# Kernel tuning notes

Measured on AMD Instinct MI355X. Metric: run time of the kernel, lower is better.

The kernel has to match this reference:

```python
import jax, jax.numpy as jnp
import numpy as np


def setup_inputs() -> dict:
    key = jax.random.key(0)
    k1, k2, k3 = jax.random.split(key, 3)
    B, IN, OUT, NCLS = 16384, 512, 1024, 5
    inputs = jax.random.normal(k1, (B, IN), dtype=jnp.float32)
    centres = jax.random.normal(k2, (OUT, IN), dtype=jnp.float32)  # nn.init.normal_(0,1)
    log_sigmas = jnp.zeros((OUT,), dtype=jnp.float32)  # constant_(0)
    # nn.Linear(out_features, 5) default init: U(-1/sqrt(fan_in), 1/sqrt(fan_in))
    bound = 1.0 / np.sqrt(OUT)
    fc_w = jax.random.uniform(k3, (NCLS, OUT), dtype=jnp.float32, minval=-bound, maxval=bound)
    fc_b = jnp.zeros((NCLS,), dtype=jnp.float32)
    return {"inputs": inputs, "centres": centres, "log_sigmas": log_sigmas,
            "fc_w": fc_w, "fc_b": fc_b}


def reference(inputs, centres, log_sigmas, fc_w, fc_b):
    # avoiding the (B, out, in) expanded intermediate the torch code builds.
    x2 = jnp.sum(inputs * inputs, axis=-1, keepdims=True)          # [B, 1]
    c2 = jnp.sum(centres * centres, axis=-1)                       # [O]
    sq = x2 + c2[None, :] - 2.0 * jnp.einsum('bi,oi->bo', inputs, centres)
    sq = jnp.maximum(sq, 0.0)                                      # [B, O]
    # distances = sqrt(sq) / exp(log_sigmas); basis = exp(-distances^2)
    dist = jnp.sqrt(sq) / jnp.exp(log_sigmas)[None, :]
    basis = jnp.exp(-(dist * dist))                                # [B, O]
    return jnp.einsum('bo,no->bn', basis, fc_w) + fc_b             # [B, 5]
```

## Files before the change

kernel.cpp:

```cpp
#include <hip/hip_runtime.h>
#include <hip/hip_bf16.h>
#include <cmath>

#define NB 16384
#define NK 512
#define NO 1024
#define NC 5
#define NSL 16

typedef float f32x4 __attribute__((ext_vector_type(4)));
typedef short s16x8 __attribute__((ext_vector_type(8)));

__device__ inline short f2bf(float f) {
    union { __hip_bfloat16 h; short s; } u;
    u.h = __float2bfloat16(f);
    return u.s;
}

__global__ void prep_bf16(const float* __restrict__ x, const float* __restrict__ c,
                          short* __restrict__ xbf, short* __restrict__ cbf,
                          float* __restrict__ x2, float* __restrict__ c2) {
    int gw   = (blockIdx.x * blockDim.x + threadIdx.x) >> 6;
    int lane = threadIdx.x & 63;
    if (gw >= NB + NO) return;
    bool isX = gw < NB;
    const float* src = isX ? (x + (size_t)gw * NK) : (c + (size_t)(gw - NB) * NK);
    short*       dst = isX ? (xbf + (size_t)gw * NK) : (cbf + (size_t)(gw - NB) * NK);
    f32x4 v0 = *(const f32x4*)(src + lane * 8);
    f32x4 v1 = *(const f32x4*)(src + lane * 8 + 4);
    s16x8 o;
    float s = 0.f;
#pragma unroll
    for (int j = 0; j < 4; ++j) {
        s += v0[j] * v0[j] + v1[j] * v1[j];
        o[j]     = f2bf(v0[j]);
        o[4 + j] = f2bf(v1[j]);
    }
    *(s16x8*)(dst + lane * 8) = o;
#pragma unroll
    for (int off = 1; off < 64; off <<= 1) s += __shfl_xor(s, off);
    if (lane == 0) {
        if (isX) x2[gw] = s;
        else     c2[gw - NB] = s;
    }
}

__global__ void prep_f32(const float* __restrict__ x, const float* __restrict__ c,
                         float* __restrict__ x2, float* __restrict__ c2) {
    int gw   = (blockIdx.x * blockDim.x + threadIdx.x) >> 6;
    int lane = threadIdx.x & 63;
    if (gw >= NB + NO) return;
    const float* src = (gw < NB) ? (x + (size_t)gw * NK)
                                 : (c + (size_t)(gw - NB) * NK);
    f32x4 v0 = *(const f32x4*)(src + lane * 8);
    f32x4 v1 = *(const f32x4*)(src + lane * 8 + 4);
    float s = 0.f;
#pragma unroll
    for (int j = 0; j < 4; ++j) s += v0[j] * v0[j] + v1[j] * v1[j];
#pragma unroll
    for (int off = 1; off < 64; off <<= 1) s += __shfl_xor(s, off);
    if (lane == 0) {
        if (gw < NB) x2[gw] = s;
        else         c2[gw - NB] = s;
    }
}

__global__ void init_out(float* __restrict__ out, const float* __restrict__ fcb) {
    int i = blockIdx.x * blockDim.x + threadIdx.x;
    if (i < NB * NC) out[i] = fcb[i % NC];
}

__global__ void reduce_out(const float* __restrict__ part,
                           const float* __restrict__ fcb,
                           float* __restrict__ out) {
    int i = blockIdx.x * blockDim.x + threadIdx.x;
    if (i >= NB * NC / 4) return;
    f32x4 s = {0.f, 0.f, 0.f, 0.f};
#pragma unroll
    for (int sl = 0; sl < NSL; ++sl)
        s += *(const f32x4*)(part + (size_t)sl * NB * NC + i * 4);
    f32x4 o;
#pragma unroll
    for (int j = 0; j < 4; ++j) o[j] = s[j] + fcb[(i * 4 + j) % NC];
    *(f32x4*)(out + i * 4) = o;
}

__device__ inline void rbf_epilogue_part(f32x4 acc[4][4],
                                         const float* __restrict__ x2,
                                         const float* __restrict__ c2,
                                         const float* __restrict__ ls,
                                         const float* __restrict__ fcw,
                                         float* __restrict__ part,
                                         int bm, int bn, int wr, int wc,
                                         int lc, int kg) {
    const int growb0 = bm * 128 + wr * 64 + kg * 4;
    const int gcol0  = bn * 128 + wc * 64 + lc;
    float* slice = part + (size_t)(bn * 2 + wc) * NB * NC;

    float c2v[4], invs2[4], w[4][5];
#pragma unroll
    for (int ni = 0; ni < 4; ++ni) {
        int gc = gcol0 + ni * 16;
        c2v[ni]   = c2[gc];
        invs2[ni] = expf(-2.f * ls[gc]);
#pragma unroll
        for (int n = 0; n < 5; ++n) w[ni][n] = fcw[n * NO + gc];
    }

#pragma unroll
    for (int mi = 0; mi < 4; ++mi) {
        float rs[4][5];
#pragma unroll
        for (int r = 0; r < 4; ++r)
#pragma unroll
            for (int n = 0; n < 5; ++n) rs[r][n] = 0.f;

#pragma unroll
        for (int r = 0; r < 4; ++r) {
            float x2v = x2[growb0 + mi * 16 + r];
#pragma unroll
            for (int ni = 0; ni < 4; ++ni) {
                float sq    = fmaxf(x2v + c2v[ni] - 2.f * acc[mi][ni][r], 0.f);
                float basis = expf(-sq * invs2[ni]);
#pragma unroll
                for (int n = 0; n < 5; ++n) rs[r][n] += basis * w[ni][n];
            }
        }
#pragma unroll
        for (int off = 1; off < 16; off <<= 1)
#pragma unroll
            for (int r = 0; r < 4; ++r)
#pragma unroll
                for (int n = 0; n < 5; ++n) rs[r][n] += __shfl_xor(rs[r][n], off);

        if (lc == 0) {
            float* dst = slice + (size_t)(growb0 + mi * 16) * NC;
            f32x4 v0 = {rs[0][0], rs[0][1], rs[0][2], rs[0][3]};
            f32x4 v1 = {rs[0][4], rs[1][0], rs[1][1], rs[1][2]};
            f32x4 v2 = {rs[1][3], rs[1][4], rs[2][0], rs[2][1]};
            f32x4 v3 = {rs[2][2], rs[2][3], rs[2][4], rs[3][0]};
            f32x4 v4 = {rs[3][1], rs[3][2], rs[3][3], rs[3][4]};
            *(f32x4*)(dst)      = v0;
            *(f32x4*)(dst + 4)  = v1;
            *(f32x4*)(dst + 8)  = v2;
            *(f32x4*)(dst + 12) = v3;
            *(f32x4*)(dst + 16) = v4;
        }
    }
}

__device__ inline void rbf_epilogue_atomic(f32x4 acc[4][4],
                                           const float* __restrict__ x2,
                                           const float* __restrict__ c2,
                                           const float* __restrict__ ls,
                                           const float* __restrict__ fcw,
                                           float* __restrict__ out,
                                           int bm, int bn, int wr, int wc,
                                           int lc, int kg) {
    const int growb0 = bm * 128 + wr * 64 + kg * 4;
    const int gcol0  = bn * 128 + wc * 64 + lc;
    float c2v[4], invs2[4], w[4][5];
#pragma unroll
    for (int ni = 0; ni < 4; ++ni) {
        int gc = gcol0 + ni * 16;
        c2v[ni]   = c2[gc];
        invs2[ni] = expf(-2.f * ls[gc]);
#pragma unroll
        for (int n = 0; n < 5; ++n) w[ni][n] = fcw[n * NO + gc];
    }
#pragma unroll
    for (int mi = 0; mi < 4; ++mi) {
        float rs[4][5];
#pragma unroll
        for (int r = 0; r < 4; ++r)
#pragma unroll
            for (int n = 0; n < 5; ++n) rs[r][n] = 0.f;
#pragma unroll
        for (int r = 0; r < 4; ++r) {
            float x2v = x2[growb0 + mi * 16 + r];
#pragma unroll
            for (int ni = 0; ni < 4; ++ni) {
                float sq    = fmaxf(x2v + c2v[ni] - 2.f * acc[mi][ni][r], 0.f);
                float basis = expf(-sq * invs2[ni]);
#pragma unroll
                for (int n = 0; n < 5; ++n) rs[r][n] += basis * w[ni][n];
            }
        }
#pragma unroll
        for (int off = 1; off < 16; off <<= 1)
#pragma unroll
            for (int r = 0; r < 4; ++r)
#pragma unroll
                for (int n = 0; n < 5; ++n) rs[r][n] += __shfl_xor(rs[r][n], off);
        if (lc == 0) {
#pragma unroll
            for (int r = 0; r < 4; ++r) {
                int grow = growb0 + mi * 16 + r;
#pragma unroll
                for (int n = 0; n < 5; ++n)
                    atomicAdd(&out[(size_t)grow * NC + n], rs[r][n]);
            }
        }
    }
}

__global__ __launch_bounds__(256)
void rbf_gemm_bf16(const short* __restrict__ Abf, const short* __restrict__ Bbf,
                   const float* __restrict__ x2, const float* __restrict__ c2,
                   const float* __restrict__ ls, const float* __restrict__ fcw,
                   float* __restrict__ part) {
    __shared__ short As[2][128 * 32];
    __shared__ short Bs[2][128 * 32];

    const int t    = threadIdx.x;
    const int lane = t & 63, wave = t >> 6;
    const int wr = wave >> 1, wc = wave & 1;
    const int lc = lane & 15, kg = lane >> 4;

    const int orig = blockIdx.x;
    const int wg   = (orig >> 3) + (orig & 7) * (1024 / 8);
    const int bm = wg >> 3, bn = wg & 7;

    const int srow = wave * 16 + (lane >> 2);
    const int scol = (lane & 3) * 8;
    const short* gA = Abf + (size_t)(bm * 128 + srow) * NK + scol;
    const short* gB = Bbf + (size_t)(bn * 128 + srow) * NK + scol;

#define STAGE(buf, kt)                                                          \
    _Pragma("unroll")                                                           \
    for (int j = 0; j < 2; ++j) {                                               \
        __builtin_amdgcn_global_load_lds(                                       \
            (const __attribute__((address_space(1))) unsigned int*)(gA + (size_t)j * 64 * NK + (kt) * 32), \
            (__attribute__((address_space(3))) unsigned int*)(&As[buf][wave * 512 + j * 2048]), \
            16, 0, 0);                                                          \
        __builtin_amdgcn_global_load_lds(                                       \
            (const __attribute__((address_space(1))) unsigned int*)(gB + (size_t)j * 64 * NK + (kt) * 32), \
            (__attribute__((address_space(3))) unsigned int*)(&Bs[buf][wave * 512 + j * 2048]), \
            16, 0, 0);                                                          \
    }

    f32x4 acc[4][4];
#pragma unroll
    for (int i = 0; i < 4; ++i)
#pragma unroll
        for (int j = 0; j < 4; ++j)
#pragma unroll
            for (int k = 0; k < 4; ++k) acc[i][j][k] = 0.f;

    const int aoff = (wr * 64 + lc) * 32 + kg * 8;
    const int boff = (wc * 64 + lc) * 32 + kg * 8;

#define COMPUTE(buf)                                                            \
    {                                                                           \
        s16x8 af[4], bfv[4];                                                    \
        _Pragma("unroll")                                                       \
        for (int mi = 0; mi < 4; ++mi) af[mi]  = *(const s16x8*)(&As[buf][aoff + mi * 512]); \
        _Pragma("unroll")                                                       \
        for (int ni = 0; ni < 4; ++ni) bfv[ni] = *(const s16x8*)(&Bs[buf][boff + ni * 512]); \
        _Pragma("unroll")                                                       \
        for (int mi = 0; mi < 4; ++mi)                                          \
            _Pragma("unroll")                                                   \
            for (int ni = 0; ni < 4; ++ni)                                      \
                acc[mi][ni] = __builtin_amdgcn_mfma_f32_16x16x32_bf16(          \
                    af[mi], bfv[ni], acc[mi][ni], 0, 0, 0);                     \
    }

    STAGE(0, 0);
    __syncthreads();
    for (int kt = 0; kt < NK / 32; kt += 2) {
        STAGE(1, kt + 1);
        COMPUTE(0);
        __syncthreads();
        if (kt + 2 < NK / 32) STAGE(0, kt + 2);
        COMPUTE(1);
        __syncthreads();
    }
#undef STAGE
#undef COMPUTE

    rbf_epilogue_part(acc, x2, c2, ls, fcw, part, bm, bn, wr, wc, lc, kg);
}

__global__ __launch_bounds__(256)
void rbf_gemm_f32(const float* __restrict__ X, const float* __restrict__ Cn,
                  const float* __restrict__ x2, const float* __restrict__ c2,
                  const float* __restrict__ ls, const float* __restrict__ fcw,
                  float* __restrict__ out) {
    __shared__ short As[128 * 40];
    __shared__ short Bs[128 * 40];

    const int t    = threadIdx.x;
    const int lane = t & 63, wave = t >> 6;
    const int wr = wave >> 1, wc = wave & 1;
    const int lc = lane & 15, kg = lane >> 4;
    const int bn = blockIdx.x & 7, bm = blockIdx.x >> 3;

    const int srow = t >> 1, shalf = t & 1;
    const float* pA = X  + (size_t)(bm * 128 + srow) * NK + shalf * 16;
    const float* pB = Cn + (size_t)(bn * 128 + srow) * NK + shalf * 16;
    const int sbase = srow * 40 + shalf * 16;

    f32x4 ra[4], rb[4];
#pragma unroll
    for (int i = 0; i < 4; ++i) {
        ra[i] = *(const f32x4*)(pA + i * 4);
        rb[i] = *(const f32x4*)(pB + i * 4);
    }

    f32x4 acc[4][4];
#pragma unroll
    for (int i = 0; i < 4; ++i)
#pragma unroll
        for (int j = 0; j < 4; ++j)
#pragma unroll
            for (int k = 0; k < 4; ++k) acc[i][j][k] = 0.f;

    const short* Ab = As + (wr * 64 + lc) * 40 + kg * 8;
    const short* Bb = Bs + (wc * 64 + lc) * 40 + kg * 8;

    for (int kt = 0; kt < NK / 32; ++kt) {
        __syncthreads();
        s16x8 va0, va1, vb0, vb1;
#pragma unroll
        for (int i = 0; i < 8; ++i) {
            va0[i] = f2bf(ra[i >> 2][i & 3]);
            va1[i] = f2bf(ra[2 + (i >> 2)][i & 3]);
            vb0[i] = f2bf(rb[i >> 2][i & 3]);
            vb1[i] = f2bf(rb[2 + (i >> 2)][i & 3]);
        }
        *(s16x8*)&As[sbase]     = va0;
        *(s16x8*)&As[sbase + 8] = va1;
        *(s16x8*)&Bs[sbase]     = vb0;
        *(s16x8*)&Bs[sbase + 8] = vb1;
        __syncthreads();

        if (kt + 1 < NK / 32) {
            const float* qA = pA + (kt + 1) * 32;
            const float* qB = pB + (kt + 1) * 32;
#pragma unroll
            for (int i = 0; i < 4; ++i) {
                ra[i] = *(const f32x4*)(qA + i * 4);
                rb[i] = *(const f32x4*)(qB + i * 4);
            }
        }

        s16x8 af[4], bfv[4];
#pragma unroll
        for (int mi = 0; mi < 4; ++mi) af[mi]  = *(const s16x8*)(Ab + mi * 16 * 40);
#pragma unroll
        for (int ni = 0; ni < 4; ++ni) bfv[ni] = *(const s16x8*)(Bb + ni * 16 * 40);
#pragma unroll
        for (int mi = 0; mi < 4; ++mi)
#pragma unroll
            for (int ni = 0; ni < 4; ++ni)
                acc[mi][ni] = __builtin_amdgcn_mfma_f32_16x16x32_bf16(
                    af[mi], bfv[ni], acc[mi][ni], 0, 0, 0);
    }

    rbf_epilogue_atomic(acc, x2, c2, ls, fcw, out, bm, bn, wr, wc, lc, kg);
}

extern "C" void kernel_launch(void* const* d_in, const int* in_sizes, int n_in,
                              void* d_out, int out_size, void* d_ws, size_t ws_size,
                              hipStream_t stream) {
    const float* X   = (const float*)d_in[0];
    const float* Cn  = (const float*)d_in[1];
    const float* ls  = (const float*)d_in[2];
    const float* fcw = (const float*)d_in[3];
    const float* fcb = (const float*)d_in[4];
    float* out = (float*)d_out;

    const size_t xbf_e  = (size_t)NB * NK;
    const size_t cbf_e  = (size_t)NO * NK;
    const size_t part_e = (size_t)NSL * NB * NC;
    const size_t need   = (xbf_e + cbf_e) * 2 + (NB + NO) * 4 + part_e * 4;

    if (ws_size >= need) {
        short* xbf  = (short*)d_ws;
        short* cbf  = xbf + xbf_e;
        float* x2   = (float*)(cbf + cbf_e);
        float* c2   = x2 + NB;
        float* part = c2 + NO;
        prep_bf16<<<(NB + NO + 3) / 4, 256, 0, stream>>>(X, Cn, xbf, cbf, x2, c2);
        rbf_gemm_bf16<<<(NO / 128) * (NB / 128), 256, 0, stream>>>(xbf, cbf, x2, c2, ls, fcw, part);
        reduce_out<<<(NB * NC / 4 + 255) / 256, 256, 0, stream>>>(part, fcb, out);
    } else {
        float* x2 = (float*)d_ws;
        float* c2 = x2 + NB;
        init_out<<<(NB * NC + 255) / 256, 256, 0, stream>>>(out, fcb);
        prep_f32<<<(NB + NO + 3) / 4, 256, 0, stream>>>(X, Cn, x2, c2);
        rbf_gemm_f32<<<(NO / 128) * (NB / 128), 256, 0, stream>>>(X, Cn, x2, c2, ls, fcw, out);
    }
}
```

Before: 130.0 us.

## Switch RBF GEMM to 256x256 tiles with 4-stage LDS pipeline

Replaces the 128x128, 4-wave, double-buffered bf16 GEMM with a 256x256-tile, 8-wave kernel that uses four LDS buffers, interleaves global-to-LDS staging with the MFMA phases, and raises wave priority around the MFMA blocks. It also XOR-swizzles the LDS layout to avoid bank conflicts and remaps workgroups for L2 locality. The epilogue is folded in and writes 16 partial slices, 4 per column block. Larger tiles cut global and LDS traffic per FLOP and the deeper pipeline hides load latency, at the cost of more registers and LDS per block, which limits occupancy.

```diff
diff --git a/kernel.cpp b/kernel.cpp
--- a/kernel.cpp
+++ b/kernel.cpp
@@ -7,6 +7,7 @@
 #define NO 1024
 #define NC 5
 #define NSL 16
+#define NT 16
 
 typedef float f32x4 __attribute__((ext_vector_type(4)));
 typedef short s16x8 __attribute__((ext_vector_type(8)));
@@ -85,17 +86,116 @@
     *(f32x4*)(out + i * 4) = o;
 }
 
-__device__ inline void rbf_epilogue_part(f32x4 acc[4][4],
-                                         const float* __restrict__ x2,
-                                         const float* __restrict__ c2,
-                                         const float* __restrict__ ls,
-                                         const float* __restrict__ fcw,
-                                         float* __restrict__ part,
-                                         int bm, int bn, int wr, int wc,
-                                         int lc, int kg) {
-    const int growb0 = bm * 128 + wr * 64 + kg * 4;
-    const int gcol0  = bn * 128 + wc * 64 + lc;
-    float* slice = part + (size_t)(bn * 2 + wc) * NB * NC;
+__global__ __launch_bounds__(512, 2)
+void rbf_gemm_256(const short* __restrict__ Abf, const short* __restrict__ Bbf,
+                  const float* __restrict__ x2, const float* __restrict__ c2,
+                  const float* __restrict__ ls, const float* __restrict__ fcw,
+                  float* __restrict__ part) {
+    __shared__ short As[4][256 * 32];
+    __shared__ short Bs[4][256 * 32];
+
+    const int t    = threadIdx.x;
+    const int lane = t & 63, wave = t >> 6;
+    const int wr  = wave >> 2, wcn = wave & 3;
+    const int lr  = lane & 15, kg  = lane >> 4;
+
+    const int orig = blockIdx.x;
+    const int wg   = (orig & 7) * 32 + (orig >> 3);
+    const int bm = wg >> 2, bn = wg & 3;
+
+    const int tc   = t ^ ((t >> 3) & 1);
+    const int srow = tc >> 2;
+    const int scol = (tc & 3) * 8;
+    const short* gA = Abf + (size_t)(bm * 256 + srow) * NK + scol;
+    const short* gB = Bbf + (size_t)(bn * 256 + srow) * NK + scol;
+
+    const int akoff = (kg * 8) ^ ((lane & 2) << 2);
+    const int arow0 = wr * 128 + lr;
+    const int brow0 = wcn * 64 + lr;
+
+    f32x4 acc[8][4];
+#pragma unroll
+    for (int i = 0; i < 8; ++i)
+#pragma unroll
+        for (int j = 0; j < 4; ++j)
+#pragma unroll
+            for (int k = 0; k < 4; ++k) acc[i][j][k] = 0.f;
+
+#define STAGE_A(kt)                                                             \
+    _Pragma("unroll")                                                           \
+    for (int j = 0; j < 2; ++j)                                                 \
+        __builtin_amdgcn_global_load_lds(                                       \
+            (const __attribute__((address_space(1))) unsigned int*)(gA + (size_t)j * 128 * NK + (kt) * 32), \
+            (__attribute__((address_space(3))) unsigned int*)(&As[(kt) & 3][j * 4096 + wave * 512]), \
+            16, 0, 0);
+
+#define STAGE_B(kt)                                                             \
+    _Pragma("unroll")                                                           \
+    for (int j = 0; j < 2; ++j)                                                 \
+        __builtin_amdgcn_global_load_lds(                                       \
+            (const __attribute__((address_space(1))) unsigned int*)(gB + (size_t)j * 128 * NK + (kt) * 32), \
+            (__attribute__((address_space(3))) unsigned int*)(&Bs[(kt) & 3][j * 4096 + wave * 512]), \
+            16, 0, 0);
+
+#define TILE_BODY(b, kt2, DOSTAGE)                                              \
+    {                                                                           \
+        const short* Ab = &As[b][0];                                            \
+        const short* Bb = &Bs[b][0];                                            \
+        s16x8 bfr[4], afr[4];                                                   \
+        _Pragma("unroll")                                                       \
+        for (int ni = 0; ni < 4; ++ni)                                          \
+            bfr[ni] = *(const s16x8*)(Bb + (brow0 + ni * 16) * 32 + akoff);     \
+        _Pragma("unroll")                                                       \
+        for (int mi = 0; mi < 4; ++mi)                                          \
+            afr[mi] = *(const s16x8*)(Ab + (arow0 + mi * 16) * 32 + akoff);     \
+        if (DOSTAGE) { STAGE_A(kt2); }                                          \
+        __builtin_amdgcn_s_setprio(1);                                          \
+        _Pragma("unroll")                                                       \
+        for (int mi = 0; mi < 4; ++mi)                                          \
+            _Pragma("unroll")                                                   \
+            for (int ni = 0; ni < 4; ++ni)                                      \
+                acc[mi][ni] = __builtin_amdgcn_mfma_f32_16x16x32_bf16(          \
+                    afr[mi], bfr[ni], acc[mi][ni], 0, 0, 0);                    \
+        __builtin_amdgcn_s_setprio(0);                                          \
+        _Pragma("unroll")                                                       \
+        for (int mi = 0; mi < 4; ++mi)                                          \
+            afr[mi] = *(const s16x8*)(Ab + (arow0 + (mi + 4) * 16) * 32 + akoff); \
+        if (DOSTAGE) { STAGE_B(kt2); }                                          \
+        __builtin_amdgcn_s_setprio(1);                                          \
+        _Pragma("unroll")                                                       \
+        for (int mi = 0; mi < 4; ++mi)                                          \
+            _Pragma("unroll")                                                   \
+            for (int ni = 0; ni < 4; ++ni)                                      \
+                acc[mi + 4][ni] = __builtin_amdgcn_mfma_f32_16x16x32_bf16(      \
+                    afr[mi], bfr[ni], acc[mi + 4][ni], 0, 0, 0);                \
+        __builtin_amdgcn_s_setprio(0);                                          \
+    }
+
+    STAGE_A(0); STAGE_B(0);
+    STAGE_A(1); STAGE_B(1);
+    asm volatile("s_waitcnt vmcnt(4)" ::: "memory");
+    __builtin_amdgcn_s_barrier();
+    __builtin_amdgcn_sched_barrier(0);
+
+    for (int kt = 0; kt < NT - 2; ++kt) {
+        TILE_BODY(kt & 3, kt + 2, true);
+        asm volatile("s_waitcnt vmcnt(4)" ::: "memory");
+        __builtin_amdgcn_s_barrier();
+        __builtin_amdgcn_sched_barrier(0);
+    }
+    TILE_BODY((NT - 2) & 3, 0, false);
+    asm volatile("s_waitcnt vmcnt(0)" ::: "memory");
+    __builtin_amdgcn_s_barrier();
+    __builtin_amdgcn_sched_barrier(0);
+    TILE_BODY((NT - 1) & 3, 0, false);
+
+#undef TILE_BODY
+#undef STAGE_A
+#undef STAGE_B
+
+    const int growb0 = bm * 256 + wr * 128 + kg * 4;
+    const int gcol0  = bn * 256 + wcn * 64 + lr;
+    float* slice = part + (size_t)(bn * 4 + wcn) * NB * NC;
 
     float c2v[4], invs2[4], w[4][5];
 #pragma unroll
@@ -108,7 +208,7 @@
     }
 
 #pragma unroll
-    for (int mi = 0; mi < 4; ++mi) {
+    for (int mi = 0; mi < 8; ++mi) {
         float rs[4][5];
 #pragma unroll
         for (int r = 0; r < 4; ++r)
@@ -133,7 +233,7 @@
 #pragma unroll
                 for (int n = 0; n < 5; ++n) rs[r][n] += __shfl_xor(rs[r][n], off);
 
-        if (lc == 0) {
+        if (lr == 0) {
             float* dst = slice + (size_t)(growb0 + mi * 16) * NC;
             f32x4 v0 = {rs[0][0], rs[0][1], rs[0][2], rs[0][3]};
             f32x4 v1 = {rs[0][4], rs[1][0], rs[1][1], rs[1][2]};
@@ -205,83 +305,6 @@
 }
 
 __global__ __launch_bounds__(256)
-void rbf_gemm_bf16(const short* __restrict__ Abf, const short* __restrict__ Bbf,
-                   const float* __restrict__ x2, const float* __restrict__ c2,
-                   const float* __restrict__ ls, const float* __restrict__ fcw,
-                   float* __restrict__ part) {
-    __shared__ short As[2][128 * 32];
-    __shared__ short Bs[2][128 * 32];
-
-    const int t    = threadIdx.x;
-    const int lane = t & 63, wave = t >> 6;
-    const int wr = wave >> 1, wc = wave & 1;
-    const int lc = lane & 15, kg = lane >> 4;
-
-    const int orig = blockIdx.x;
-    const int wg   = (orig >> 3) + (orig & 7) * (1024 / 8);
-    const int bm = wg >> 3, bn = wg & 7;
-
-    const int srow = wave * 16 + (lane >> 2);
-    const int scol = (lane & 3) * 8;
-    const short* gA = Abf + (size_t)(bm * 128 + srow) * NK + scol;
-    const short* gB = Bbf + (size_t)(bn * 128 + srow) * NK + scol;
-
-#define STAGE(buf, kt)                                                          \
-    _Pragma("unroll")                                                           \
-    for (int j = 0; j < 2; ++j) {                                               \
-        __builtin_amdgcn_global_load_lds(                                       \
-            (const __attribute__((address_space(1))) unsigned int*)(gA + (size_t)j * 64 * NK + (kt) * 32), \
-            (__attribute__((address_space(3))) unsigned int*)(&As[buf][wave * 512 + j * 2048]), \
-            16, 0, 0);                                                          \
-        __builtin_amdgcn_global_load_lds(                                       \
-            (const __attribute__((address_space(1))) unsigned int*)(gB + (size_t)j * 64 * NK + (kt) * 32), \
-            (__attribute__((address_space(3))) unsigned int*)(&Bs[buf][wave * 512 + j * 2048]), \
-            16, 0, 0);                                                          \
-    }
-
-    f32x4 acc[4][4];
-#pragma unroll
-    for (int i = 0; i < 4; ++i)
-#pragma unroll
-        for (int j = 0; j < 4; ++j)
-#pragma unroll
-            for (int k = 0; k < 4; ++k) acc[i][j][k] = 0.f;
-
-    const int aoff = (wr * 64 + lc) * 32 + kg * 8;
-    const int boff = (wc * 64 + lc) * 32 + kg * 8;
-
-#define COMPUTE(buf)                                                            \
-    {                                                                           \
-        s16x8 af[4], bfv[4];                                                    \
-        _Pragma("unroll")                                                       \
-        for (int mi = 0; mi < 4; ++mi) af[mi]  = *(const s16x8*)(&As[buf][aoff + mi * 512]); \
-        _Pragma("unroll")                                                       \
-        for (int ni = 0; ni < 4; ++ni) bfv[ni] = *(const s16x8*)(&Bs[buf][boff + ni * 512]); \
-        _Pragma("unroll")                                                       \
-        for (int mi = 0; mi < 4; ++mi)                                          \
-            _Pragma("unroll")                                                   \
-            for (int ni = 0; ni < 4; ++ni)                                      \
-                acc[mi][ni] = __builtin_amdgcn_mfma_f32_16x16x32_bf16(          \
-                    af[mi], bfv[ni], acc[mi][ni], 0, 0, 0);                     \
-    }
-
-    STAGE(0, 0);
-    __syncthreads();
-    for (int kt = 0; kt < NK / 32; kt += 2) {
-        STAGE(1, kt + 1);
-        COMPUTE(0);
-        __syncthreads();
-        if (kt + 2 < NK / 32) STAGE(0, kt + 2);
-        COMPUTE(1);
-        __syncthreads();
-    }
-#undef STAGE
-#undef COMPUTE
-
-    rbf_epilogue_part(acc, x2, c2, ls, fcw, part, bm, bn, wr, wc, lc, kg);
-}
-
-__global__ __launch_bounds__(256)
 void rbf_gemm_f32(const float* __restrict__ X, const float* __restrict__ Cn,
                   const float* __restrict__ x2, const float* __restrict__ c2,
                   const float* __restrict__ ls, const float* __restrict__ fcw,
@@ -382,7 +405,7 @@
         float* c2   = x2 + NB;
         float* part = c2 + NO;
         prep_bf16<<<(NB + NO + 3) / 4, 256, 0, stream>>>(X, Cn, xbf, cbf, x2, c2);
-        rbf_gemm_bf16<<<(NO / 128) * (NB / 128), 256, 0, stream>>>(xbf, cbf, x2, c2, ls, fcw, part);
+        rbf_gemm_256<<<(NB / 256) * (NO / 256), 512, 0, stream>>>(xbf, cbf, x2, c2, ls, fcw, part);
         reduce_out<<<(NB * NC / 4 + 255) / 256, 256, 0, stream>>>(part, fcb, out);
     } else {
         float* x2 = (float*)d_ws;
```

Measured after the change: 122.6 us. 5.7% less time.

## Use 256x128 block tile with 512 threads, swizzled LDS and MFMA priority

Applied to the files above, without the earlier changes.

Replaces the 128x128, 256-thread bf16 GEMM with a 256x128 tile run by 8 waves, so each B tile is loaded once for twice as many rows. The LDS load addresses are XOR-swizzled to cut bank conflicts, and s_setprio is raised around the MFMA block. The loop uses a single-barrier double-buffered schedule with a different workgroup remapping. The fused RBF epilogue is inlined into the new kernel. Larger blocks halve the grid and may reduce occupancy or hurt load balance.

```diff
diff --git a/kernel.cpp b/kernel.cpp
--- a/kernel.cpp
+++ b/kernel.cpp
@@ -7,9 +7,12 @@
 #define NO 1024
 #define NC 5
 #define NSL 16
+#define NT 16
 
 typedef float f32x4 __attribute__((ext_vector_type(4)));
 typedef short s16x8 __attribute__((ext_vector_type(8)));
+#define AS1 __attribute__((address_space(1)))
+#define AS3 __attribute__((address_space(3)))
 
 __device__ inline short f2bf(float f) {
     union { __hip_bfloat16 h; short s; } u;
@@ -85,17 +88,83 @@
     *(f32x4*)(out + i * 4) = o;
 }
 
-__device__ inline void rbf_epilogue_part(f32x4 acc[4][4],
-                                         const float* __restrict__ x2,
-                                         const float* __restrict__ c2,
-                                         const float* __restrict__ ls,
-                                         const float* __restrict__ fcw,
-                                         float* __restrict__ part,
-                                         int bm, int bn, int wr, int wc,
-                                         int lc, int kg) {
-    const int growb0 = bm * 128 + wr * 64 + kg * 4;
-    const int gcol0  = bn * 128 + wc * 64 + lc;
-    float* slice = part + (size_t)(bn * 2 + wc) * NB * NC;
+__global__ __launch_bounds__(512, 4)
+void rbf_gemm_512(const short* __restrict__ Abf, const short* __restrict__ Bbf,
+                  const float* __restrict__ x2, const float* __restrict__ c2,
+                  const float* __restrict__ ls, const float* __restrict__ fcw,
+                  float* __restrict__ part) {
+    __shared__ short As[2][256 * 32];
+    __shared__ short Bs[2][128 * 32];
+
+    const int t    = threadIdx.x;
+    const int lane = t & 63;
+    const int wave = t >> 6;
+    const int wr   = wave >> 1, wcn = wave & 1;
+    const int lr   = lane & 15, kg  = lane >> 4;
+
+    const int orig = blockIdx.x;
+    const int wg   = (orig & 7) * 64 + (orig >> 3);
+    const int bm = wg >> 3, bn = wg & 7;
+
+    const int l0   = t ^ ((t >> 3) & 3);
+    const int srow = l0 >> 2;
+    const int kc8  = (l0 & 3) * 8;
+    const short* gA0 = Abf + (size_t)(bm * 256 + srow) * NK + kc8;
+    const short* gA1 = gA0 + (size_t)128 * NK;
+    const short* gB0 = Bbf + (size_t)(bn * 128 + srow) * NK + kc8;
+
+#define STAGE(buf, kt) do {                                                     \
+    __builtin_amdgcn_global_load_lds(                                           \
+        (const AS1 unsigned int*)(gA0 + (kt) * 32),                             \
+        (AS3 unsigned int*)(&As[buf][(size_t)t * 8]), 16, 0, 0);                \
+    __builtin_amdgcn_global_load_lds(                                           \
+        (const AS1 unsigned int*)(gA1 + (kt) * 32),                             \
+        (AS3 unsigned int*)(&As[buf][(size_t)(512 + t) * 8]), 16, 0, 0);        \
+    __builtin_amdgcn_global_load_lds(                                           \
+        (const AS1 unsigned int*)(gB0 + (kt) * 32),                             \
+        (AS3 unsigned int*)(&Bs[buf][(size_t)t * 8]), 16, 0, 0);                \
+} while (0)
+
+    const int akoff = (kg ^ ((lr >> 1) & 3)) * 8;
+    const int arow0 = (wr * 64 + lr) * 32;
+    const int brow0 = (wcn * 64 + lr) * 32;
+
+    f32x4 acc[4][4];
+#pragma unroll
+    for (int i = 0; i < 4; ++i)
+#pragma unroll
+        for (int j = 0; j < 4; ++j)
+#pragma unroll
+            for (int k = 0; k < 4; ++k) acc[i][j][k] = 0.f;
+
+    STAGE(0, 0);
+    __syncthreads();
+#pragma unroll
+    for (int kt = 0; kt < NT; ++kt) {
+        const int buf = kt & 1;
+        if (kt + 1 < NT) STAGE(buf ^ 1, kt + 1);
+        s16x8 af[4], bfv[4];
+#pragma unroll
+        for (int ni = 0; ni < 4; ++ni)
+            bfv[ni] = *(const s16x8*)(&Bs[buf][brow0 + ni * 512 + akoff]);
+#pragma unroll
+        for (int mi = 0; mi < 4; ++mi)
+            af[mi]  = *(const s16x8*)(&As[buf][arow0 + mi * 512 + akoff]);
+        __builtin_amdgcn_s_setprio(1);
+#pragma unroll
+        for (int mi = 0; mi < 4; ++mi)
+#pragma unroll
+            for (int ni = 0; ni < 4; ++ni)
+                acc[mi][ni] = __builtin_amdgcn_mfma_f32_16x16x32_bf16(
+                    af[mi], bfv[ni], acc[mi][ni], 0, 0, 0);
+        __builtin_amdgcn_s_setprio(0);
+        if (kt + 1 < NT) __syncthreads();
+    }
+#undef STAGE
+
+    const int growb0 = bm * 256 + wr * 64 + kg * 4;
+    const int gcol0  = bn * 128 + wcn * 64 + lr;
+    float* slice = part + (size_t)(bn * 2 + wcn) * NB * NC;
 
     float c2v[4], invs2[4], w[4][5];
 #pragma unroll
@@ -133,7 +202,7 @@
 #pragma unroll
                 for (int n = 0; n < 5; ++n) rs[r][n] += __shfl_xor(rs[r][n], off);
 
-        if (lc == 0) {
+        if (lr == 0) {
             float* dst = slice + (size_t)(growb0 + mi * 16) * NC;
             f32x4 v0 = {rs[0][0], rs[0][1], rs[0][2], rs[0][3]};
             f32x4 v1 = {rs[0][4], rs[1][0], rs[1][1], rs[1][2]};
@@ -205,83 +274,6 @@
 }
 
 __global__ __launch_bounds__(256)
-void rbf_gemm_bf16(const short* __restrict__ Abf, const short* __restrict__ Bbf,
-                   const float* __restrict__ x2, const float* __restrict__ c2,
-                   const float* __restrict__ ls, const float* __restrict__ fcw,
-                   float* __restrict__ part) {
-    __shared__ short As[2][128 * 32];
-    __shared__ short Bs[2][128 * 32];
-
-    const int t    = threadIdx.x;
-    const int lane = t & 63, wave = t >> 6;
-    const int wr = wave >> 1, wc = wave & 1;
-    const int lc = lane & 15, kg = lane >> 4;
-
-    const int orig = blockIdx.x;
-    const int wg   = (orig >> 3) + (orig & 7) * (1024 / 8);
-    const int bm = wg >> 3, bn = wg & 7;
-
-    const int srow = wave * 16 + (lane >> 2);
-    const int scol = (lane & 3) * 8;
-    const short* gA = Abf + (size_t)(bm * 128 + srow) * NK + scol;
-    const short* gB = Bbf + (size_t)(bn * 128 + srow) * NK + scol;
-
-#define STAGE(buf, kt)                                                          \
-    _Pragma("unroll")                                                           \
-    for (int j = 0; j < 2; ++j) {                                               \
-        __builtin_amdgcn_global_load_lds(                                       \
-            (const __attribute__((address_space(1))) unsigned int*)(gA + (size_t)j * 64 * NK + (kt) * 32), \
-            (__attribute__((address_space(3))) unsigned int*)(&As[buf][wave * 512 + j * 2048]), \
-            16, 0, 0);                                                          \
-        __builtin_amdgcn_global_load_lds(                                       \
-            (const __attribute__((address_space(1))) unsigned int*)(gB + (size_t)j * 64 * NK + (kt) * 32), \
-            (__attribute__((address_space(3))) unsigned int*)(&Bs[buf][wave * 512 + j * 2048]), \
-            16, 0, 0);                                                          \
-    }
-
-    f32x4 acc[4][4];
-#pragma unroll
-    for (int i = 0; i < 4; ++i)
-#pragma unroll
-        for (int j = 0; j < 4; ++j)
-#pragma unroll
-            for (int k = 0; k < 4; ++k) acc[i][j][k] = 0.f;
-
-    const int aoff = (wr * 64 + lc) * 32 + kg * 8;
-    const int boff = (wc * 64 + lc) * 32 + kg * 8;
-
-#define COMPUTE(buf)                                                            \
-    {                                                                           \
-        s16x8 af[4], bfv[4];                                                    \
-        _Pragma("unroll")                                                       \
-        for (int mi = 0; mi < 4; ++mi) af[mi]  = *(const s16x8*)(&As[buf][aoff + mi * 512]); \
-        _Pragma("unroll")                                                       \
-        for (int ni = 0; ni < 4; ++ni) bfv[ni] = *(const s16x8*)(&Bs[buf][boff + ni * 512]); \
-        _Pragma("unroll")                                                       \
-        for (int mi = 0; mi < 4; ++mi)                                          \
-            _Pragma("unroll")                                                   \
-            for (int ni = 0; ni < 4; ++ni)                                      \
-                acc[mi][ni] = __builtin_amdgcn_mfma_f32_16x16x32_bf16(          \
-                    af[mi], bfv[ni], acc[mi][ni], 0, 0, 0);                     \
-    }
-
-    STAGE(0, 0);
-    __syncthreads();
-    for (int kt = 0; kt < NK / 32; kt += 2) {
-        STAGE(1, kt + 1);
-        COMPUTE(0);
-        __syncthreads();
-        if (kt + 2 < NK / 32) STAGE(0, kt + 2);
-        COMPUTE(1);
-        __syncthreads();
-    }
-#undef STAGE
-#undef COMPUTE
-
-    rbf_epilogue_part(acc, x2, c2, ls, fcw, part, bm, bn, wr, wc, lc, kg);
-}
-
-__global__ __launch_bounds__(256)
 void rbf_gemm_f32(const float* __restrict__ X, const float* __restrict__ Cn,
                   const float* __restrict__ x2, const float* __restrict__ c2,
                   const float* __restrict__ ls, const float* __restrict__ fcw,
@@ -382,7 +374,7 @@
         float* c2   = x2 + NB;
         float* part = c2 + NO;
         prep_bf16<<<(NB + NO + 3) / 4, 256, 0, stream>>>(X, Cn, xbf, cbf, x2, c2);
-        rbf_gemm_bf16<<<(NO / 128) * (NB / 128), 256, 0, stream>>>(xbf, cbf, x2, c2, ls, fcw, part);
+        rbf_gemm_512<<<(NB / 256) * (NO / 128), 512, 0, stream>>>(xbf, cbf, x2, c2, ls, fcw, part);
         reduce_out<<<(NB * NC / 4 + 255) / 256, 256, 0, stream>>>(part, fcb, out);
     } else {
         float* x2 = (float*)d_ws;
```

After: 124.7 us. 1.04x faster.
